# Kernel optimization log

Measured on AMD Instinct MI355X. Metric: run time of the kernel, lower is better.

The kernel has to match this reference:

```python
import jax, jax.numpy as jnp
import numpy as np

TEMPERATURE = 0.07
NORM_EPS = 1e-12   # F.normalize eps
LOG_EPS = 1e-08


def setup_inputs() -> dict:
    key = jax.random.key(0)
    k1, k2 = jax.random.split(key)
    N, D, C = 8192, 512, 64
    projections = jax.random.normal(k1, (N, D), dtype=jnp.float32)
    targets = jax.random.randint(k2, (N,), 0, C, dtype=jnp.int64)
    return {"projections": projections, "targets": targets}


def reference(projections, targets):
    # L2-normalize rows (matches F.normalize: x / max(||x||, eps))
    norm = jnp.linalg.norm(projections, axis=1, keepdims=True)
    p = projections / jnp.maximum(norm, NORM_EPS)

    # [N, N] cosine similarity / temperature
    sim = jnp.matmul(p, p.T) / TEMPERATURE
    # row-max subtraction for numerical stability (gradient flows through max,
    # as in the torch original)
    sim = sim - jnp.max(sim, axis=1, keepdims=True)
    exp_sim = jnp.exp(sim)

    n = projections.shape[0]
    eye = jnp.eye(n, dtype=bool)
    mask_self = ~eye                                   # exclude self-pairs
    mask_pos = (targets[:, None] == targets[None, :]) & mask_self

    denom = jnp.sum(jnp.where(mask_self, exp_sim, 0.0), axis=1, keepdims=True)
    log_prob = sim - jnp.log(denom + LOG_EPS)

    num = jnp.sum(jnp.where(mask_pos, log_prob, 0.0), axis=1)
    cnt = jnp.sum(mask_pos, axis=1).astype(log_prob.dtype)
    # divide_no_nan: 0 where cnt == 0
    loss_per_sample = jnp.where(cnt == 0, 0.0, num / jnp.where(cnt == 0, 1.0, cnt))
    return loss_per_sample
```

## Files before the change

kernel.cpp:

```cpp
#include <hip/hip_runtime.h>
#include <hip/hip_bf16.h>
#include <math.h>

#define N_ROWS 8192
#define DIM    512
#define NCLS   64
#define BM     128
#define BK     32
#define NKT    (DIM / BK)
#define NTILE  (N_ROWS / BM)
#define NTRI   (NTILE * (NTILE + 1) / 2)
#define M_CONST 14.285714285714286f
#define SCALE_SQRT 3.7796447300922722f

using bf16x8 = __attribute__((ext_vector_type(8))) short;
using f32x4  = __attribute__((ext_vector_type(4))) float;

static __device__ inline unsigned short f2bf(float x) {
  unsigned u = __float_as_uint(x);
  unsigned r = u + 0x7FFFu + ((u >> 16) & 1u);
  return (unsigned short)(r >> 16);
}

__global__ __launch_bounds__(256) void normalize_rows(const float* __restrict__ proj,
                                                      unsigned short* __restrict__ outb) {
  const int row  = blockIdx.x * 4 + (threadIdx.x >> 6);
  const int lane = threadIdx.x & 63;
  const float4* src = (const float4*)(proj + (size_t)row * DIM);
  float4 a = src[lane * 2];
  float4 b = src[lane * 2 + 1];
  float ss = a.x*a.x + a.y*a.y + a.z*a.z + a.w*a.w
           + b.x*b.x + b.y*b.y + b.z*b.z + b.w*b.w;
#pragma unroll
  for (int off = 1; off < 64; off <<= 1) ss += __shfl_xor(ss, off);
  const float scale = SCALE_SQRT / fmaxf(sqrtf(ss), 1e-12f);
  float v[8] = {a.x, a.y, a.z, a.w, b.x, b.y, b.z, b.w};
  unsigned short h[8];
#pragma unroll
  for (int i = 0; i < 8; ++i) h[i] = f2bf(v[i] * scale);
  uint4 packed;
  packed.x = (unsigned)h[0] | ((unsigned)h[1] << 16);
  packed.y = (unsigned)h[2] | ((unsigned)h[3] << 16);
  packed.z = (unsigned)h[4] | ((unsigned)h[5] << 16);
  packed.w = (unsigned)h[6] | ((unsigned)h[7] << 16);
  *(uint4*)(outb + (size_t)row * DIM + lane * 8) = packed;
}

__global__ __launch_bounds__(1024) void class_hist(const int* __restrict__ tgt,
                                                   int* __restrict__ hist) {
  __shared__ int h[16][NCLS];
  const int wid = threadIdx.x >> 6;
  const int lane = threadIdx.x & 63;
  if (lane < NCLS) h[wid][lane] = 0;
  __syncthreads();
  for (int i = threadIdx.x; i < N_ROWS; i += 1024) atomicAdd(&h[wid][tgt[i]], 1);
  __syncthreads();
  if (threadIdx.x < NCLS) {
    int s = 0;
#pragma unroll
    for (int w = 0; w < 16; ++w) s += h[w][threadIdx.x];
    hist[threadIdx.x] = s;
  }
}

__global__ __launch_bounds__(256, 4) void supcon_tile(const unsigned short* __restrict__ p16,
                                                      const int* __restrict__ tgt,
                                                      float* __restrict__ dpart,
                                                      float* __restrict__ spart) {
  const int logical = (blockIdx.x & 7) * (NTRI / 8) + (blockIdx.x >> 3);
  int rem = logical, br = 0;
  while (rem >= NTILE - br) { rem -= NTILE - br; ++br; }
  const int bc = br + rem;

  __shared__ short As[2][BM * BK];
  __shared__ short Bs[2][BM * BK];
  __shared__ int tgr[BM], tgc[BM];

  const int tid  = threadIdx.x;
  const int lane = tid & 63;
  const int wid  = tid >> 6;
  const int wr = wid >> 1, wc = wid & 1;
  const int lhi = lane >> 4, llo = lane & 15;

  const size_t rowA0 = (size_t)br * BM;
  const size_t rowB0 = (size_t)bc * BM;

  const int r_st  = lane >> 2;
  const int gp_st = lane & 3;

#define STAGE(BUF, KT) do {                                                          \
  _Pragma("unroll")                                                                  \
  for (int c = 0; c < 2; ++c) {                                                      \
    const int m  = wid + 4 * c;                               \
    const int r  = m * 16 + r_st;                                                    \
    const int gl = gp_st ^ ((r >> 1) & 3);          \
    const unsigned short* gA = p16 + (rowA0 + r) * DIM + (KT) * BK + gl * 8;         \
    const unsigned short* gB = p16 + (rowB0 + r) * DIM + (KT) * BK + gl * 8;         \
    __builtin_amdgcn_global_load_lds((const __attribute__((address_space(1))) void*)gA, \
        (__attribute__((address_space(3))) void*)&As[BUF][r * BK + gp_st * 8], 16, 0, 0); \
    __builtin_amdgcn_global_load_lds((const __attribute__((address_space(1))) void*)gB, \
        (__attribute__((address_space(3))) void*)&Bs[BUF][r * BK + gp_st * 8], 16, 0, 0); \
  }                                                                                  \
} while (0)

  STAGE(0, 0);
  if (tid < BM)            tgr[tid] = tgt[br * BM + tid];
  else if (tid < 2 * BM)   tgc[tid - BM] = tgt[bc * BM + (tid - BM)];

  f32x4 zero = {0.f, 0.f, 0.f, 0.f};
  f32x4 acc[4][4];
#pragma unroll
  for (int i = 0; i < 4; ++i)
#pragma unroll
    for (int j = 0; j < 4; ++j) acc[i][j] = zero;

  __syncthreads();

  int cur = 0;
  for (int kt = 0; kt < NKT; ++kt) {
    if (kt + 1 < NKT) STAGE(cur ^ 1, kt + 1);
    bf16x8 af[4], bfr[4];
#pragma unroll
    for (int mi = 0; mi < 4; ++mi) {
      const int Ra = wr * 64 + mi * 16 + llo;
      af[mi] = *(const bf16x8*)&As[cur][Ra * BK + ((lhi ^ ((Ra >> 1) & 3)) * 8)];
    }
#pragma unroll
    for (int ni = 0; ni < 4; ++ni) {
      const int Rb = wc * 64 + ni * 16 + llo;
      bfr[ni] = *(const bf16x8*)&Bs[cur][Rb * BK + ((lhi ^ ((Rb >> 1) & 3)) * 8)];
    }
#pragma unroll
    for (int mi = 0; mi < 4; ++mi)
#pragma unroll
      for (int ni = 0; ni < 4; ++ni)
        acc[mi][ni] = __builtin_amdgcn_mfma_f32_16x16x32_bf16(af[mi], bfr[ni], acc[mi][ni], 0, 0, 0);
    __syncthreads();
    cur ^= 1;
  }
#undef STAGE

  const bool diag = (br == bc);
  float ecol[4] = {0.f, 0.f, 0.f, 0.f};
  float scol[4] = {0.f, 0.f, 0.f, 0.f};

#pragma unroll
  for (int mi = 0; mi < 4; ++mi) {
#pragma unroll
    for (int rg = 0; rg < 4; ++rg) {
      const int rin  = wr * 64 + mi * 16 + lhi * 4 + rg;
      const int trow = tgr[rin];
      float esum = 0.f, ssum = 0.f;
#pragma unroll
      for (int ni = 0; ni < 4; ++ni) {
        const int cin = wc * 64 + ni * 16 + llo;
        const float sim = acc[mi][ni][rg];
        const bool self = diag && (rin == cin);
        const float e = self ? 0.f : __expf(sim - M_CONST);
        const bool pos = (!self) && (trow == tgc[cin]);
        const float sv = pos ? sim : 0.f;
        esum += e;  ssum += sv;
        ecol[ni] += e;  scol[ni] += sv;
      }
#pragma unroll
      for (int off = 1; off < 16; off <<= 1) {
        esum += __shfl_xor(esum, off);
        ssum += __shfl_xor(ssum, off);
      }
      if (llo == 0) {
        const int grow = br * BM + rin;
        dpart[(size_t)(bc * 2 + wc) * N_ROWS + grow] = esum;
        spart[(size_t)(bc * 2 + wc) * N_ROWS + grow] = ssum;
      }
    }
  }

  if (!diag) {
#pragma unroll
    for (int ni = 0; ni < 4; ++ni) {
      float ec = ecol[ni], sc = scol[ni];
      ec += __shfl_xor(ec, 16); ec += __shfl_xor(ec, 32);
      sc += __shfl_xor(sc, 16); sc += __shfl_xor(sc, 32);
      if (lhi == 0) {
        const int gcol = bc * BM + wc * 64 + ni * 16 + llo;
        dpart[(size_t)(br * 2 + wr) * N_ROWS + gcol] = ec;
        spart[(size_t)(br * 2 + wr) * N_ROWS + gcol] = sc;
      }
    }
  }
}

__global__ __launch_bounds__(256) void combine_loss(const float* __restrict__ dpart,
                                                    const float* __restrict__ spart,
                                                    const int* __restrict__ tgt,
                                                    const int* __restrict__ hist,
                                                    float* __restrict__ out) {
  __shared__ float dsh[4][64], ssh[4][64];
  const int lane = threadIdx.x & 63;
  const int g    = threadIdx.x >> 6;
  const int r    = blockIdx.x * 64 + lane;
  float d = 0.f, s = 0.f;
  for (int k = g * 32; k < g * 32 + 32; ++k) {
    d += dpart[(size_t)k * N_ROWS + r];
    s += spart[(size_t)k * N_ROWS + r];
  }
  dsh[g][lane] = d; ssh[g][lane] = s;
  __syncthreads();
  if (g == 0) {
    d = dsh[0][lane] + dsh[1][lane] + dsh[2][lane] + dsh[3][lane];
    s = ssh[0][lane] + ssh[1][lane] + ssh[2][lane] + ssh[3][lane];
    const int cnt = hist[tgt[r]] - 1;
    out[r] = (cnt > 0) ? (s / (float)cnt - M_CONST - logf(d + 1e-8f)) : 0.f;
  }
}

extern "C" void kernel_launch(void* const* d_in, const int* in_sizes, int n_in,
                              void* d_out, int out_size, void* d_ws, size_t ws_size,
                              hipStream_t stream) {
  const float* proj = (const float*)d_in[0];
  const int*   tgt  = (const int*)d_in[1];
  float* out = (float*)d_out;

  char* ws = (char*)d_ws;
  unsigned short* p16  = (unsigned short*)ws;
  float* dpart = (float*)(ws + (size_t)8  * 1024 * 1024);
  float* spart = (float*)(ws + (size_t)12 * 1024 * 1024);
  int*   hist  = (int*)(ws + (size_t)16 * 1024 * 1024);

  normalize_rows<<<N_ROWS / 4, 256, 0, stream>>>(proj, p16);
  class_hist<<<1, 1024, 0, stream>>>(tgt, hist);
  supcon_tile<<<NTRI, 256, 0, stream>>>(p16, tgt, dpart, spart);
  combine_loss<<<N_ROWS / 64, 256, 0, stream>>>(dpart, spart, tgt, hist, out);
}
```

Measured before the change: 97.71 us.

## Use 512-thread tiles with BK=64, in-block partial reduction, exp2 scaling, fused histogram

The tile kernel now runs 8 waves of 512 threads, each computing 64x32 outputs, with a doubled K-step of 64 and a new XOR swizzle. Per-wave row and column partials are reduced in shared memory, so each tile writes one slot per row instead of two, which halves the partial buffers read by the combine kernel. Scaling by log2(e) is folded into the normalization so the epilogue can use the hardware exp2 directly. The class histogram moves into the normalize kernel through global atomics after a memset, which replaces a separate single-block launch. The cost is more LDS per block, an extra barrier, and per-row atomic contention on 64 counters.

```diff
diff --git a/kernel.cpp b/kernel.cpp
--- a/kernel.cpp
+++ b/kernel.cpp
@@ -6,12 +6,15 @@
 #define DIM    512
 #define NCLS   64
 #define BM     128
-#define BK     32
+#define BK     64
 #define NKT    (DIM / BK)
 #define NTILE  (N_ROWS / BM)
 #define NTRI   (NTILE * (NTILE + 1) / 2)
+#define NSLOT  NTILE
 #define M_CONST 14.285714285714286f
-#define SCALE_SQRT 3.7796447300922722f
+#define L2E     1.4426950408889634f
+#define M2_CONST 20.60992915555662f
+#define SCALE2  4.539815541256959f
 
 using bf16x8 = __attribute__((ext_vector_type(8))) short;
 using f32x4  = __attribute__((ext_vector_type(4))) float;
@@ -23,9 +26,12 @@
 }
 
 __global__ __launch_bounds__(256) void normalize_rows(const float* __restrict__ proj,
-                                                      unsigned short* __restrict__ outb) {
+                                                      const int* __restrict__ tgt,
+                                                      unsigned short* __restrict__ outb,
+                                                      int* __restrict__ hist) {
   const int row  = blockIdx.x * 4 + (threadIdx.x >> 6);
   const int lane = threadIdx.x & 63;
+  if (lane == 0) atomicAdd(&hist[tgt[row]], 1);
   const float4* src = (const float4*)(proj + (size_t)row * DIM);
   float4 a = src[lane * 2];
   float4 b = src[lane * 2 + 1];
@@ -33,7 +39,7 @@
            + b.x*b.x + b.y*b.y + b.z*b.z + b.w*b.w;
 #pragma unroll
   for (int off = 1; off < 64; off <<= 1) ss += __shfl_xor(ss, off);
-  const float scale = SCALE_SQRT / fmaxf(sqrtf(ss), 1e-12f);
+  const float scale = SCALE2 / fmaxf(sqrtf(ss), 1e-12f);
   float v[8] = {a.x, a.y, a.z, a.w, b.x, b.y, b.z, b.w};
   unsigned short h[8];
 #pragma unroll
@@ -46,61 +52,43 @@
   *(uint4*)(outb + (size_t)row * DIM + lane * 8) = packed;
 }
 
-__global__ __launch_bounds__(1024) void class_hist(const int* __restrict__ tgt,
-                                                   int* __restrict__ hist) {
-  __shared__ int h[16][NCLS];
-  const int wid = threadIdx.x >> 6;
-  const int lane = threadIdx.x & 63;
-  if (lane < NCLS) h[wid][lane] = 0;
-  __syncthreads();
-  for (int i = threadIdx.x; i < N_ROWS; i += 1024) atomicAdd(&h[wid][tgt[i]], 1);
-  __syncthreads();
-  if (threadIdx.x < NCLS) {
-    int s = 0;
-#pragma unroll
-    for (int w = 0; w < 16; ++w) s += h[w][threadIdx.x];
-    hist[threadIdx.x] = s;
-  }
-}
-
-__global__ __launch_bounds__(256, 4) void supcon_tile(const unsigned short* __restrict__ p16,
+__global__ __launch_bounds__(512, 4) void supcon_tile(const unsigned short* __restrict__ p16,
                                                       const int* __restrict__ tgt,
                                                       float* __restrict__ dpart,
                                                       float* __restrict__ spart) {
-  const int logical = (blockIdx.x & 7) * (NTRI / 8) + (blockIdx.x >> 3);
+  const int logical = ((int)blockIdx.x & 7) * (NTRI / 8) + ((int)blockIdx.x >> 3);
   int rem = logical, br = 0;
   while (rem >= NTILE - br) { rem -= NTILE - br; ++br; }
   const int bc = br + rem;
 
   __shared__ short As[2][BM * BK];
   __shared__ short Bs[2][BM * BK];
-  __shared__ int tgr[BM], tgc[BM];
+  __shared__ int   tgr[BM], tgc[BM];
+  __shared__ float redE[4][BM], redS[4][BM];
+  __shared__ float redEc[2][BM], redSc[2][BM];
 
   const int tid  = threadIdx.x;
   const int lane = tid & 63;
   const int wid  = tid >> 6;
-  const int wr = wid >> 1, wc = wid & 1;
+  const int wm = wid >> 2, wn = wid & 3;
   const int lhi = lane >> 4, llo = lane & 15;
 
   const size_t rowA0 = (size_t)br * BM;
   const size_t rowB0 = (size_t)bc * BM;
 
-  const int r_st  = lane >> 2;
-  const int gp_st = lane & 3;
-
-#define STAGE(BUF, KT) do {                                                          \
-  _Pragma("unroll")                                                                  \
-  for (int c = 0; c < 2; ++c) {                                                      \
-    const int m  = wid + 4 * c;                               \
-    const int r  = m * 16 + r_st;                                                    \
-    const int gl = gp_st ^ ((r >> 1) & 3);          \
-    const unsigned short* gA = p16 + (rowA0 + r) * DIM + (KT) * BK + gl * 8;         \
-    const unsigned short* gB = p16 + (rowB0 + r) * DIM + (KT) * BK + gl * 8;         \
-    __builtin_amdgcn_global_load_lds((const __attribute__((address_space(1))) void*)gA, \
-        (__attribute__((address_space(3))) void*)&As[BUF][r * BK + gp_st * 8], 16, 0, 0); \
-    __builtin_amdgcn_global_load_lds((const __attribute__((address_space(1))) void*)gB, \
-        (__attribute__((address_space(3))) void*)&Bs[BUF][r * BK + gp_st * 8], 16, 0, 0); \
-  }                                                                                  \
+#define STAGE(BUF, KT) do {                                                         \
+  _Pragma("unroll")                                                                 \
+  for (int j = 0; j < 2; ++j) {                                                     \
+    const int g  = tid + j * 512;                                                   \
+    const int r  = g >> 3, gp = g & 7;                                              \
+    const int gl = gp ^ (r & 7);                                                    \
+    const unsigned short* sA = p16 + (rowA0 + r) * DIM + (KT) * BK + gl * 8;        \
+    const unsigned short* sB = p16 + (rowB0 + r) * DIM + (KT) * BK + gl * 8;        \
+    __builtin_amdgcn_global_load_lds((const __attribute__((address_space(1))) void*)sA, \
+        (__attribute__((address_space(3))) void*)&As[BUF][g * 8], 16, 0, 0);        \
+    __builtin_amdgcn_global_load_lds((const __attribute__((address_space(1))) void*)sB, \
+        (__attribute__((address_space(3))) void*)&Bs[BUF][g * 8], 16, 0, 0);        \
+  }                                                                                 \
 } while (0)
 
   STAGE(0, 0);
@@ -108,57 +96,62 @@
   else if (tid < 2 * BM)   tgc[tid - BM] = tgt[bc * BM + (tid - BM)];
 
   f32x4 zero = {0.f, 0.f, 0.f, 0.f};
-  f32x4 acc[4][4];
+  f32x4 acc[4][2];
 #pragma unroll
   for (int i = 0; i < 4; ++i)
 #pragma unroll
-    for (int j = 0; j < 4; ++j) acc[i][j] = zero;
+    for (int j = 0; j < 2; ++j) acc[i][j] = zero;
 
   __syncthreads();
 
   int cur = 0;
   for (int kt = 0; kt < NKT; ++kt) {
     if (kt + 1 < NKT) STAGE(cur ^ 1, kt + 1);
-    bf16x8 af[4], bfr[4];
-#pragma unroll
-    for (int mi = 0; mi < 4; ++mi) {
-      const int Ra = wr * 64 + mi * 16 + llo;
-      af[mi] = *(const bf16x8*)&As[cur][Ra * BK + ((lhi ^ ((Ra >> 1) & 3)) * 8)];
+#pragma unroll
+    for (int ks = 0; ks < 2; ++ks) {
+      bf16x8 af[4], bfr[2];
+#pragma unroll
+      for (int mi = 0; mi < 4; ++mi) {
+        const int Ra = wm * 64 + mi * 16 + llo;
+        af[mi] = *(const bf16x8*)&As[cur][Ra * BK + (((ks * 4 + lhi) ^ (Ra & 7)) * 8)];
+      }
+#pragma unroll
+      for (int ni = 0; ni < 2; ++ni) {
+        const int Rb = wn * 32 + ni * 16 + llo;
+        bfr[ni] = *(const bf16x8*)&Bs[cur][Rb * BK + (((ks * 4 + lhi) ^ (Rb & 7)) * 8)];
+      }
+#pragma unroll
+      for (int mi = 0; mi < 4; ++mi)
+#pragma unroll
+        for (int ni = 0; ni < 2; ++ni)
+          acc[mi][ni] = __builtin_amdgcn_mfma_f32_16x16x32_bf16(af[mi], bfr[ni], acc[mi][ni], 0, 0, 0);
     }
-#pragma unroll
-    for (int ni = 0; ni < 4; ++ni) {
-      const int Rb = wc * 64 + ni * 16 + llo;
-      bfr[ni] = *(const bf16x8*)&Bs[cur][Rb * BK + ((lhi ^ ((Rb >> 1) & 3)) * 8)];
-    }
-#pragma unroll
-    for (int mi = 0; mi < 4; ++mi)
-#pragma unroll
-      for (int ni = 0; ni < 4; ++ni)
-        acc[mi][ni] = __builtin_amdgcn_mfma_f32_16x16x32_bf16(af[mi], bfr[ni], acc[mi][ni], 0, 0, 0);
     __syncthreads();
     cur ^= 1;
   }
 #undef STAGE
 
   const bool diag = (br == bc);
-  float ecol[4] = {0.f, 0.f, 0.f, 0.f};
-  float scol[4] = {0.f, 0.f, 0.f, 0.f};
+  const int tc0 = tgc[wn * 32 + llo];
+  const int tc1 = tgc[wn * 32 + 16 + llo];
+  float ecol[2] = {0.f, 0.f};
+  float scol[2] = {0.f, 0.f};
 
 #pragma unroll
   for (int mi = 0; mi < 4; ++mi) {
 #pragma unroll
     for (int rg = 0; rg < 4; ++rg) {
-      const int rin  = wr * 64 + mi * 16 + lhi * 4 + rg;
+      const int rin  = wm * 64 + mi * 16 + lhi * 4 + rg;
       const int trow = tgr[rin];
       float esum = 0.f, ssum = 0.f;
 #pragma unroll
-      for (int ni = 0; ni < 4; ++ni) {
-        const int cin = wc * 64 + ni * 16 + llo;
-        const float sim = acc[mi][ni][rg];
+      for (int ni = 0; ni < 2; ++ni) {
+        const int cin = wn * 32 + ni * 16 + llo;
+        const float x = acc[mi][ni][rg];
         const bool self = diag && (rin == cin);
-        const float e = self ? 0.f : __expf(sim - M_CONST);
-        const bool pos = (!self) && (trow == tgc[cin]);
-        const float sv = pos ? sim : 0.f;
+        const float e = self ? 0.f : __builtin_amdgcn_exp2f(x - M2_CONST);
+        const bool pos = (!self) && (trow == (ni ? tc1 : tc0));
+        const float sv = pos ? x : 0.f;
         esum += e;  ssum += sv;
         ecol[ni] += e;  scol[ni] += sv;
       }
@@ -167,26 +160,32 @@
         esum += __shfl_xor(esum, off);
         ssum += __shfl_xor(ssum, off);
       }
-      if (llo == 0) {
-        const int grow = br * BM + rin;
-        dpart[(size_t)(bc * 2 + wc) * N_ROWS + grow] = esum;
-        spart[(size_t)(bc * 2 + wc) * N_ROWS + grow] = ssum;
-      }
+      if (llo == 0) { redE[wn][rin] = esum; redS[wn][rin] = ssum; }
     }
   }
-
   if (!diag) {
 #pragma unroll
-    for (int ni = 0; ni < 4; ++ni) {
+    for (int ni = 0; ni < 2; ++ni) {
       float ec = ecol[ni], sc = scol[ni];
       ec += __shfl_xor(ec, 16); ec += __shfl_xor(ec, 32);
       sc += __shfl_xor(sc, 16); sc += __shfl_xor(sc, 32);
       if (lhi == 0) {
-        const int gcol = bc * BM + wc * 64 + ni * 16 + llo;
-        dpart[(size_t)(br * 2 + wr) * N_ROWS + gcol] = ec;
-        spart[(size_t)(br * 2 + wr) * N_ROWS + gcol] = sc;
+        redEc[wm][wn * 32 + ni * 16 + llo] = ec;
+        redSc[wm][wn * 32 + ni * 16 + llo] = sc;
       }
     }
+  }
+  __syncthreads();
+
+  if (tid < BM) {
+    const float e = redE[0][tid] + redE[1][tid] + redE[2][tid] + redE[3][tid];
+    const float s = redS[0][tid] + redS[1][tid] + redS[2][tid] + redS[3][tid];
+    dpart[(size_t)bc * N_ROWS + rowA0 + tid] = e;
+    spart[(size_t)bc * N_ROWS + rowA0 + tid] = s;
+  } else if (tid < 2 * BM && !diag) {
+    const int c = tid - BM;
+    dpart[(size_t)br * N_ROWS + rowB0 + c] = redEc[0][c] + redEc[1][c];
+    spart[(size_t)br * N_ROWS + rowB0 + c] = redSc[0][c] + redSc[1][c];
   }
 }
 
@@ -200,7 +199,7 @@
   const int g    = threadIdx.x >> 6;
   const int r    = blockIdx.x * 64 + lane;
   float d = 0.f, s = 0.f;
-  for (int k = g * 32; k < g * 32 + 32; ++k) {
+  for (int k = g * (NSLOT / 4); k < (g + 1) * (NSLOT / 4); ++k) {
     d += dpart[(size_t)k * N_ROWS + r];
     s += spart[(size_t)k * N_ROWS + r];
   }
@@ -210,7 +209,7 @@
     d = dsh[0][lane] + dsh[1][lane] + dsh[2][lane] + dsh[3][lane];
     s = ssh[0][lane] + ssh[1][lane] + ssh[2][lane] + ssh[3][lane];
     const int cnt = hist[tgt[r]] - 1;
-    out[r] = (cnt > 0) ? (s / (float)cnt - M_CONST - logf(d + 1e-8f)) : 0.f;
+    out[r] = (cnt > 0) ? (s / (L2E * (float)cnt) - M_CONST - logf(d + 1e-8f)) : 0.f;
   }
 }
 
@@ -224,11 +223,11 @@
   char* ws = (char*)d_ws;
   unsigned short* p16  = (unsigned short*)ws;
   float* dpart = (float*)(ws + (size_t)8  * 1024 * 1024);
-  float* spart = (float*)(ws + (size_t)12 * 1024 * 1024);
-  int*   hist  = (int*)(ws + (size_t)16 * 1024 * 1024);
-
-  normalize_rows<<<N_ROWS / 4, 256, 0, stream>>>(proj, p16);
-  class_hist<<<1, 1024, 0, stream>>>(tgt, hist);
-  supcon_tile<<<NTRI, 256, 0, stream>>>(p16, tgt, dpart, spart);
+  float* spart = (float*)(ws + (size_t)10 * 1024 * 1024);
+  int*   hist  = (int*)(ws + (size_t)12 * 1024 * 1024);
+
+  (void)hipMemsetAsync(hist, 0, NCLS * sizeof(int), stream);
+  normalize_rows<<<N_ROWS / 4, 256, 0, stream>>>(proj, tgt, p16, hist);
+  supcon_tile<<<NTRI, 512, 0, stream>>>(p16, tgt, dpart, spart);
   combine_loss<<<N_ROWS / 64, 256, 0, stream>>>(dpart, spart, tgt, hist, out);
 }
```

After: 125.9 us. 1.29x slower.
